# Kernel optimization log

Measured on AMD Instinct MI355X. Metric: run time of the kernel, lower is better.

Reference implementation:

```python
import jax, jax.numpy as jnp
import numpy as np

# FTRL-FM hyperparameters (from option dict)
L1_1 = 0.05   # regularizer_l1_1st
L2_1 = 0.05   # regularizer_l2_1st (source sets it equal to l1_1st)
L1_2 = 0.05   # regularizer_l1_2nd
L2_2 = 1.0    # regularizer_l2_2nd
ALPHA1, BETA1 = 0.1, 1.0
ALPHA2, BETA2 = 0.1, 1.0

B, K, F, M = 4096, 50, 1_000_000, 32


def setup_inputs() -> dict:
    key = jax.random.key(0)
    k1, k2, k3, k4, k5 = jax.random.split(key, 5)
    x_idx = jax.random.randint(k1, (B, K), 0, F)                      # active feature indices
    z_1st = jax.random.normal(k2, (F,), dtype=jnp.float32) * 0.3
    n_1st = jax.random.uniform(k3, (F,), dtype=jnp.float32) * 10.0 + 0.1
    z_2nd = jax.random.normal(k4, (F, M), dtype=jnp.float32) * jnp.float32(np.sqrt(0.1))
    n_2nd = jax.random.uniform(k5, (F, M), dtype=jnp.float32) * 10.0 + 0.1
    return {"x_idx": x_idx, "z_1st": z_1st, "n_1st": n_1st,
            "z_2nd": z_2nd, "n_2nd": n_2nd}


def _ftrl_weight(z, n, l1, l2, alpha, beta, sign_scale):
    # FTRL lazy weight: 0 inside L1 ball, else (sign(z)*sign_scale - z) / ((beta+sqrt(n))/alpha + l2)
    sign = jnp.where(z >= 0, 1.0, -1.0).astype(z.dtype)
    denom = (beta + jnp.sqrt(n)) / alpha + l2
    w = (sign * sign_scale - z) / denom
    return jnp.where(jnp.abs(z) <= l1, jnp.zeros_like(w), w)


def reference(x_idx, z_1st, n_1st, z_2nd, n_2nd):
    # Gather per-sample active-feature FTRL state (irregular memory access)
    z1 = z_1st[x_idx]            # [B, K]
    n1 = n_1st[x_idx]            # [B, K]
    z2 = z_2nd[x_idx]            # [B, K, M]
    n2 = n_2nd[x_idx]            # [B, K, M]

    # 1st-order lazy weights; linear term w_1st.dot(x) with binary x
    w1 = _ftrl_weight(z1, n1, L1_1, L2_1, ALPHA1, BETA1, L1_1)
    lin = jnp.sum(w1, axis=-1)   # [B]

    # 2nd-order lazy weights; source numerator uses sign * regularizer_l2_1st
    w2 = _ftrl_weight(z2, n2, L1_2, L2_2, ALPHA2, BETA2, L2_1)

    # FM pairwise sum_{i<j} <w2_i, w2_j> = 0.5 * (||sum_i w2_i||^2 - sum_i ||w2_i||^2)
    s = jnp.sum(w2, axis=1)                       # [B, M]
    pair = 0.5 * (jnp.sum(s * s, axis=-1) - jnp.sum(w2 * w2, axis=(1, 2)))  # [B]

    return lin + pair
```

## Files before the change

kernel.cpp:

```cpp
#include <hip/hip_runtime.h>
#include <cstddef>


namespace {
constexpr int KF = 50;
constexpr int MF = 32;

__device__ __forceinline__ float ftrl_w(float z, float n, float l1, float l2,
                                        float ss ) {
  float sgn = (z >= 0.f) ? 1.f : -1.f;
  float denom = (1.0f + sqrtf(n)) * 10.0f + l2;
  float w = (sgn * ss - z) / denom;
  return (fabsf(z) <= l1) ? 0.f : w;
}
}

__global__ __launch_bounds__(256) void ftrl_fm_kernel(
    const int* __restrict__ x_idx,
    const float* __restrict__ z1t, const float* __restrict__ n1t,
    const float* __restrict__ z2t, const float* __restrict__ n2t,
    float* __restrict__ out, int B) {
  const int wave_in_block = threadIdx.x >> 6;
  const int b = blockIdx.x * (blockDim.x >> 6) + wave_in_block;
  if (b >= B) return;
  const int lane = threadIdx.x & 63;
  const int* row = x_idx + b * KF;

  const int myidx = row[lane < KF ? lane : 0];

  float lin = 0.f;
  if (lane < KF) {
    float z = z1t[myidx];
    float n = n1t[myidx];
    lin = ftrl_w(z, n, 0.05f, 0.05f, 0.05f);
  }

  const int m4 = lane & 7;
  const int kp = lane >> 3;
  float4 s = make_float4(0.f, 0.f, 0.f, 0.f);
  float sumsq = 0.f;

#pragma unroll
  for (int kk = 0; kk < 7; ++kk) {
    const int k = kk * 8 + kp;
    const bool act = (k < KF);
    const int idx = __shfl(myidx, act ? k : 0, 64);
    if (act) {
      const float4 z = *((const float4*)(z2t + (size_t)idx * MF) + m4);
      const float4 n = *((const float4*)(n2t + (size_t)idx * MF) + m4);
      float w;
      w = ftrl_w(z.x, n.x, 0.05f, 1.0f, 0.05f); s.x += w; sumsq += w * w;
      w = ftrl_w(z.y, n.y, 0.05f, 1.0f, 0.05f); s.y += w; sumsq += w * w;
      w = ftrl_w(z.z, n.z, 0.05f, 1.0f, 0.05f); s.z += w; sumsq += w * w;
      w = ftrl_w(z.w, n.w, 0.05f, 1.0f, 0.05f); s.w += w; sumsq += w * w;
    }
  }

#pragma unroll
  for (int off = 8; off < 64; off <<= 1) {
    s.x += __shfl_xor(s.x, off, 64);
    s.y += __shfl_xor(s.y, off, 64);
    s.z += __shfl_xor(s.z, off, 64);
    s.w += __shfl_xor(s.w, off, 64);
  }

  float v = lin
          + (s.x * s.x + s.y * s.y + s.z * s.z + s.w * s.w) * (1.0f / 16.0f)
          - 0.5f * sumsq;

#pragma unroll
  for (int off = 1; off < 64; off <<= 1)
    v += __shfl_xor(v, off, 64);

  if (lane == 0) out[b] = v;
}

extern "C" void kernel_launch(void* const* d_in, const int* in_sizes, int n_in,
                              void* d_out, int out_size, void* d_ws, size_t ws_size,
                              hipStream_t stream) {
  const int*   x_idx = (const int*)d_in[0];
  const float* z1t   = (const float*)d_in[1];
  const float* n1t   = (const float*)d_in[2];
  const float* z2t   = (const float*)d_in[3];
  const float* n2t   = (const float*)d_in[4];
  float* out = (float*)d_out;

  const int B = out_size;
  const int waves_per_block = 4;
  const int grid = (B + waves_per_block - 1) / waves_per_block;
  ftrl_fm_kernel<<<grid, 256, 0, stream>>>(x_idx, z1t, n1t, z2t, n2t, out, B);
}
```

Before: 24.12 us.

## Spread each sample across a full 256-thread block with shared-memory reduction

```diff
diff --git a/kernel.cpp b/kernel.cpp
--- a/kernel.cpp
+++ b/kernel.cpp
@@ -13,47 +13,60 @@
   float w = (sgn * ss - z) / denom;
   return (fabsf(z) <= l1) ? 0.f : w;
 }
+
+__device__ __forceinline__ float dot4(const float4& a, const float4& b) {
+  return a.x * b.x + a.y * b.y + a.z * b.z + a.w * b.w;
+}
 }
 
 __global__ __launch_bounds__(256) void ftrl_fm_kernel(
     const int* __restrict__ x_idx,
     const float* __restrict__ z1t, const float* __restrict__ n1t,
     const float* __restrict__ z2t, const float* __restrict__ n2t,
-    float* __restrict__ out, int B) {
-  const int wave_in_block = threadIdx.x >> 6;
-  const int b = blockIdx.x * (blockDim.x >> 6) + wave_in_block;
-  if (b >= B) return;
-  const int lane = threadIdx.x & 63;
-  const int* row = x_idx + b * KF;
+    float* __restrict__ out) {
+  const int b = blockIdx.x;
+  const int tid = threadIdx.x;
+  const int wave = tid >> 6;
+  const int lane = tid & 63;
+  const int m4 = lane & 7;
+  const int g = wave * 8 + (lane >> 3);
 
-  const int myidx = row[lane < KF ? lane : 0];
+  const int* __restrict__ row = x_idx + b * KF;
+
+  const int idx0 = row[g];
+  const int k1 = g + 32;
+  const bool act1 = (k1 < KF);
+  const int idx1 = row[act1 ? k1 : 0];
+  const float actf = act1 ? 1.f : 0.f;
+
+  const float4 z0 = *((const float4*)(z2t + (size_t)idx0 * MF) + m4);
+  const float4 n0 = *((const float4*)(n2t + (size_t)idx0 * MF) + m4);
+  const float4 z1 = *((const float4*)(z2t + (size_t)idx1 * MF) + m4);
+  const float4 n1 = *((const float4*)(n2t + (size_t)idx1 * MF) + m4);
 
   float lin = 0.f;
-  if (lane < KF) {
-    float z = z1t[myidx];
-    float n = n1t[myidx];
-    lin = ftrl_w(z, n, 0.05f, 0.05f, 0.05f);
+  if (tid < KF) {
+    const int i1 = row[tid];
+    lin = ftrl_w(z1t[i1], n1t[i1], 0.05f, 0.05f, 0.05f);
   }
 
-  const int m4 = lane & 7;
-  const int kp = lane >> 3;
-  float4 s = make_float4(0.f, 0.f, 0.f, 0.f);
-  float sumsq = 0.f;
-
-#pragma unroll
-  for (int kk = 0; kk < 7; ++kk) {
-    const int k = kk * 8 + kp;
-    const bool act = (k < KF);
-    const int idx = __shfl(myidx, act ? k : 0, 64);
-    if (act) {
-      const float4 z = *((const float4*)(z2t + (size_t)idx * MF) + m4);
-      const float4 n = *((const float4*)(n2t + (size_t)idx * MF) + m4);
-      float w;
-      w = ftrl_w(z.x, n.x, 0.05f, 1.0f, 0.05f); s.x += w; sumsq += w * w;
-      w = ftrl_w(z.y, n.y, 0.05f, 1.0f, 0.05f); s.y += w; sumsq += w * w;
-      w = ftrl_w(z.z, n.z, 0.05f, 1.0f, 0.05f); s.z += w; sumsq += w * w;
-      w = ftrl_w(z.w, n.w, 0.05f, 1.0f, 0.05f); s.w += w; sumsq += w * w;
-    }
+  float4 s;
+  float sumsq;
+  {
+    float wx = ftrl_w(z0.x, n0.x, 0.05f, 1.0f, 0.05f);
+    float wy = ftrl_w(z0.y, n0.y, 0.05f, 1.0f, 0.05f);
+    float wz = ftrl_w(z0.z, n0.z, 0.05f, 1.0f, 0.05f);
+    float ww = ftrl_w(z0.w, n0.w, 0.05f, 1.0f, 0.05f);
+    s = make_float4(wx, wy, wz, ww);
+    sumsq = wx * wx + wy * wy + wz * wz + ww * ww;
+  }
+  {
+    float wx = actf * ftrl_w(z1.x, n1.x, 0.05f, 1.0f, 0.05f);
+    float wy = actf * ftrl_w(z1.y, n1.y, 0.05f, 1.0f, 0.05f);
+    float wz = actf * ftrl_w(z1.z, n1.z, 0.05f, 1.0f, 0.05f);
+    float ww = actf * ftrl_w(z1.w, n1.w, 0.05f, 1.0f, 0.05f);
+    s.x += wx; s.y += wy; s.z += wz; s.w += ww;
+    sumsq += wx * wx + wy * wy + wz * wz + ww * ww;
   }
 
 #pragma unroll
@@ -64,15 +77,32 @@
     s.w += __shfl_xor(s.w, off, 64);
   }
 
-  float v = lin
-          + (s.x * s.x + s.y * s.y + s.z * s.z + s.w * s.w) * (1.0f / 16.0f)
-          - 0.5f * sumsq;
+  __shared__ float4 sArr[4][8];
+  __shared__ float partial[4];
+  if (lane < 8) sArr[wave][lane] = s;
 
+  float v = lin - 0.5f * sumsq;
 #pragma unroll
   for (int off = 1; off < 64; off <<= 1)
     v += __shfl_xor(v, off, 64);
+  if (lane == 0) partial[wave] = v;
 
-  if (lane == 0) out[b] = v;
+  __syncthreads();
+
+  if (tid == 0) {
+    float acc = partial[0] + partial[1] + partial[2] + partial[3];
+    float sq = 0.f;
+#pragma unroll
+    for (int m = 0; m < 8; ++m) {
+      float4 t = sArr[0][m];
+      t.x += sArr[1][m].x + sArr[2][m].x + sArr[3][m].x;
+      t.y += sArr[1][m].y + sArr[2][m].y + sArr[3][m].y;
+      t.z += sArr[1][m].z + sArr[2][m].z + sArr[3][m].z;
+      t.w += sArr[1][m].w + sArr[2][m].w + sArr[3][m].w;
+      sq += dot4(t, t);
+    }
+    out[b] = acc + 0.5f * sq;
+  }
 }
 
 extern "C" void kernel_launch(void* const* d_in, const int* in_sizes, int n_in,
@@ -86,7 +116,5 @@
   float* out = (float*)d_out;
 
   const int B = out_size;
-  const int waves_per_block = 4;
-  const int grid = (B + waves_per_block - 1) / waves_per_block;
-  ftrl_fm_kernel<<<grid, 256, 0, stream>>>(x_idx, z1t, n1t, z2t, n2t, out, B);
+  ftrl_fm_kernel<<<B, 256, 0, stream>>>(x_idx, z1t, n1t, z2t, n2t, out);
 }
```

After: 21.58 us. 1.12x faster.

## Split each sample's features across a block's waves and process two samples per block

Applied to the files above, without the earlier changes.

```diff
diff --git a/kernel.cpp b/kernel.cpp
--- a/kernel.cpp
+++ b/kernel.cpp
@@ -20,59 +20,124 @@
     const float* __restrict__ z1t, const float* __restrict__ n1t,
     const float* __restrict__ z2t, const float* __restrict__ n2t,
     float* __restrict__ out, int B) {
-  const int wave_in_block = threadIdx.x >> 6;
-  const int b = blockIdx.x * (blockDim.x >> 6) + wave_in_block;
-  if (b >= B) return;
-  const int lane = threadIdx.x & 63;
-  const int* row = x_idx + b * KF;
+  const int tid = threadIdx.x;
+  const int wave = tid >> 6;
+  const int lane = tid & 63;
+  const int m4 = lane & 7;
+  const int g = wave * 8 + (lane >> 3);
+  const int k1 = g + 32;
+  const bool act1 = (k1 < KF);
+  const float actf = act1 ? 1.f : 0.f;
+  const int kc = act1 ? k1 : g;
 
-  const int myidx = row[lane < KF ? lane : 0];
+  const int b0 = blockIdx.x;
+  const int b1 = b0 + gridDim.x;
+  const bool has1 = (b1 < B);
 
-  float lin = 0.f;
-  if (lane < KF) {
-    float z = z1t[myidx];
-    float n = n1t[myidx];
-    lin = ftrl_w(z, n, 0.05f, 0.05f, 0.05f);
+  const int* __restrict__ row0 = x_idx + (size_t)b0 * KF;
+  const int* __restrict__ row1 = x_idx + (size_t)(has1 ? b1 : b0) * KF;
+
+  const int a0 = row0[g];
+  const int a1 = row0[kc];
+  const int c0 = row1[g];
+  const int c1 = row1[kc];
+  const int tfeat = (tid < KF) ? tid : 0;
+  const int i1a = row0[tfeat];
+  const int i1b = row1[tfeat];
+
+  const float4* __restrict__ z2v = (const float4*)z2t;
+  const float4* __restrict__ n2v = (const float4*)n2t;
+  const float4 Az0 = z2v[a0 * 8 + m4];
+  const float4 An0 = n2v[a0 * 8 + m4];
+  const float4 Az1 = z2v[a1 * 8 + m4];
+  const float4 An1 = n2v[a1 * 8 + m4];
+  const float4 Cz0 = z2v[c0 * 8 + m4];
+  const float4 Cn0 = n2v[c0 * 8 + m4];
+  const float4 Cz1 = z2v[c1 * 8 + m4];
+  const float4 Cn1 = n2v[c1 * 8 + m4];
+
+  const float z1a = z1t[i1a], n1a = n1t[i1a];
+  const float z1b = z1t[i1b], n1b = n1t[i1b];
+
+  __shared__ float sMem[2][4][32];
+  __shared__ float pMem[2][4];
+
+  {
+    float wx = ftrl_w(Az0.x, An0.x, 0.05f, 1.0f, 0.05f);
+    float wy = ftrl_w(Az0.y, An0.y, 0.05f, 1.0f, 0.05f);
+    float wz = ftrl_w(Az0.z, An0.z, 0.05f, 1.0f, 0.05f);
+    float ww = ftrl_w(Az0.w, An0.w, 0.05f, 1.0f, 0.05f);
+    float4 s = make_float4(wx, wy, wz, ww);
+    float sumsq = wx * wx + wy * wy + wz * wz + ww * ww;
+    wx = actf * ftrl_w(Az1.x, An1.x, 0.05f, 1.0f, 0.05f);
+    wy = actf * ftrl_w(Az1.y, An1.y, 0.05f, 1.0f, 0.05f);
+    wz = actf * ftrl_w(Az1.z, An1.z, 0.05f, 1.0f, 0.05f);
+    ww = actf * ftrl_w(Az1.w, An1.w, 0.05f, 1.0f, 0.05f);
+    s.x += wx; s.y += wy; s.z += wz; s.w += ww;
+    sumsq += wx * wx + wy * wy + wz * wz + ww * ww;
+
+#pragma unroll
+    for (int off = 8; off < 64; off <<= 1) {
+      s.x += __shfl_xor(s.x, off, 64);
+      s.y += __shfl_xor(s.y, off, 64);
+      s.z += __shfl_xor(s.z, off, 64);
+      s.w += __shfl_xor(s.w, off, 64);
+    }
+    if (lane < 8) *(float4*)&sMem[0][wave][lane * 4] = s;
+
+    float v = ((tid < KF) ? ftrl_w(z1a, n1a, 0.05f, 0.05f, 0.05f) : 0.f)
+            - 0.5f * sumsq;
+#pragma unroll
+    for (int off = 1; off < 64; off <<= 1) v += __shfl_xor(v, off, 64);
+    if (lane == 0) pMem[0][wave] = v;
   }
 
-  const int m4 = lane & 7;
-  const int kp = lane >> 3;
-  float4 s = make_float4(0.f, 0.f, 0.f, 0.f);
-  float sumsq = 0.f;
+  {
+    float wx = ftrl_w(Cz0.x, Cn0.x, 0.05f, 1.0f, 0.05f);
+    float wy = ftrl_w(Cz0.y, Cn0.y, 0.05f, 1.0f, 0.05f);
+    float wz = ftrl_w(Cz0.z, Cn0.z, 0.05f, 1.0f, 0.05f);
+    float ww = ftrl_w(Cz0.w, Cn0.w, 0.05f, 1.0f, 0.05f);
+    float4 s = make_float4(wx, wy, wz, ww);
+    float sumsq = wx * wx + wy * wy + wz * wz + ww * ww;
+    wx = actf * ftrl_w(Cz1.x, Cn1.x, 0.05f, 1.0f, 0.05f);
+    wy = actf * ftrl_w(Cz1.y, Cn1.y, 0.05f, 1.0f, 0.05f);
+    wz = actf * ftrl_w(Cz1.z, Cn1.z, 0.05f, 1.0f, 0.05f);
+    ww = actf * ftrl_w(Cz1.w, Cn1.w, 0.05f, 1.0f, 0.05f);
+    s.x += wx; s.y += wy; s.z += wz; s.w += ww;
+    sumsq += wx * wx + wy * wy + wz * wz + ww * ww;
 
 #pragma unroll
-  for (int kk = 0; kk < 7; ++kk) {
-    const int k = kk * 8 + kp;
-    const bool act = (k < KF);
-    const int idx = __shfl(myidx, act ? k : 0, 64);
-    if (act) {
-      const float4 z = *((const float4*)(z2t + (size_t)idx * MF) + m4);
-      const float4 n = *((const float4*)(n2t + (size_t)idx * MF) + m4);
-      float w;
-      w = ftrl_w(z.x, n.x, 0.05f, 1.0f, 0.05f); s.x += w; sumsq += w * w;
-      w = ftrl_w(z.y, n.y, 0.05f, 1.0f, 0.05f); s.y += w; sumsq += w * w;
-      w = ftrl_w(z.z, n.z, 0.05f, 1.0f, 0.05f); s.z += w; sumsq += w * w;
-      w = ftrl_w(z.w, n.w, 0.05f, 1.0f, 0.05f); s.w += w; sumsq += w * w;
+    for (int off = 8; off < 64; off <<= 1) {
+      s.x += __shfl_xor(s.x, off, 64);
+      s.y += __shfl_xor(s.y, off, 64);
+      s.z += __shfl_xor(s.z, off, 64);
+      s.w += __shfl_xor(s.w, off, 64);
+    }
+    if (lane < 8) *(float4*)&sMem[1][wave][lane * 4] = s;
+
+    float v = ((tid < KF) ? ftrl_w(z1b, n1b, 0.05f, 0.05f, 0.05f) : 0.f)
+            - 0.5f * sumsq;
+#pragma unroll
+    for (int off = 1; off < 64; off <<= 1) v += __shfl_xor(v, off, 64);
+    if (lane == 0) pMem[1][wave] = v;
+  }
+
+  __syncthreads();
+
+  if (wave < 2) {
+    const int sb = wave;
+    float sm = 0.f;
+    if (lane < 32)
+      sm = sMem[sb][0][lane] + sMem[sb][1][lane] + sMem[sb][2][lane] + sMem[sb][3][lane];
+    float sq = sm * sm;
+#pragma unroll
+    for (int off = 1; off < 32; off <<= 1) sq += __shfl_xor(sq, off, 64);
+    if (lane == 0) {
+      const float acc = pMem[sb][0] + pMem[sb][1] + pMem[sb][2] + pMem[sb][3];
+      if (sb == 0) out[b0] = acc + 0.5f * sq;
+      else if (has1) out[b1] = acc + 0.5f * sq;
     }
   }
-
-#pragma unroll
-  for (int off = 8; off < 64; off <<= 1) {
-    s.x += __shfl_xor(s.x, off, 64);
-    s.y += __shfl_xor(s.y, off, 64);
-    s.z += __shfl_xor(s.z, off, 64);
-    s.w += __shfl_xor(s.w, off, 64);
-  }
-
-  float v = lin
-          + (s.x * s.x + s.y * s.y + s.z * s.z + s.w * s.w) * (1.0f / 16.0f)
-          - 0.5f * sumsq;
-
-#pragma unroll
-  for (int off = 1; off < 64; off <<= 1)
-    v += __shfl_xor(v, off, 64);
-
-  if (lane == 0) out[b] = v;
 }
 
 extern "C" void kernel_launch(void* const* d_in, const int* in_sizes, int n_in,
@@ -86,7 +151,6 @@
   float* out = (float*)d_out;
 
   const int B = out_size;
-  const int waves_per_block = 4;
-  const int grid = (B + waves_per_block - 1) / waves_per_block;
+  const int grid = (B + 1) / 2;
   ftrl_fm_kernel<<<grid, 256, 0, stream>>>(x_idx, z1t, n1t, z2t, n2t, out, B);
 }
```

Result: faster. 21.98 us (median of 2 runs) (-8.9%).
